# Optimization experiments

Hardware: AMD Instinct MI355X
Metric: run time of the kernel (lower is better)

## Reference

```python
import jax, jax.numpy as jnp
import numpy as np

N_EMBD = 2048
N_HEAD = 16
HEAD_DIM = N_EMBD // N_HEAD
B, T = 4, 2048
EPS = 1e-5


def layer_norm(x, w, b):
    mu = jnp.mean(x, axis=-1, keepdims=True)
    var = jnp.var(x, axis=-1, keepdims=True)
    return (x - mu) * jax.lax.rsqrt(var + EPS) * w + b


def setup_inputs() -> dict:
    key = jax.random.key(0)
    ks = jax.random.split(key, 8)
    s = 0.02
    return {
        "x": jax.random.normal(ks[0], (B, T, N_EMBD), dtype=jnp.float32),
        "ln1_w": jnp.ones((N_EMBD,), jnp.float32),
        "ln1_b": jnp.zeros((N_EMBD,), jnp.float32),
        "attn_w": jax.random.normal(ks[1], (N_EMBD, 3 * N_EMBD), jnp.float32) * s,
        "attn_b": jnp.zeros((3 * N_EMBD,), jnp.float32),
        "ln2_w": jnp.ones((N_EMBD,), jnp.float32),
        "ln2_b": jnp.zeros((N_EMBD,), jnp.float32),
        "fc_w": jax.random.normal(ks[2], (N_EMBD, 4 * N_EMBD), jnp.float32) * s,
        "fc_b": jnp.zeros((4 * N_EMBD,), jnp.float32),
        "proj_w": jax.random.normal(ks[3], (4 * N_EMBD, N_EMBD), jnp.float32) * s,
        "proj_b": jnp.zeros((N_EMBD,), jnp.float32),
    }


def reference(x, ln1_w, ln1_b, attn_w, attn_b, ln2_w, ln2_b, fc_w, fc_b, proj_w, proj_b):
    b, t, c = x.shape
    # --- causal self-attention on ln_1(x); note: source Block has NO residual
    # and attention's c_proj is never invoked in the original forward. ---
    h = layer_norm(x, ln1_w, ln1_b)
    qkv = h @ attn_w + attn_b                      # [B,T,3C]
    q, k, v = jnp.split(qkv, 3, axis=-1)
    q = q.reshape(b, t, N_HEAD, HEAD_DIM)
    k = k.reshape(b, t, N_HEAD, HEAD_DIM)
    v = v.reshape(b, t, N_HEAD, HEAD_DIM)
    scale = 1.0 / np.sqrt(HEAD_DIM).astype(np.float32)
    scores = jnp.einsum("bqhd,bkhd->bhqk", q, k) * scale   # [B,H,T,T]
    causal = jnp.tril(jnp.ones((t, t), dtype=bool))
    scores = jnp.where(causal, scores, -jnp.inf)
    attn = jax.nn.softmax(scores, axis=-1)
    y = jnp.einsum("bhqk,bkhd->bqhd", attn, v).reshape(b, t, c)
    # --- MLP on ln_2(y); again no residual in the source Block ---
    h2 = layer_norm(y, ln2_w, ln2_b)
    out = jax.nn.gelu(h2 @ fc_w + fc_b, approximate=False) @ proj_w + proj_b
    return out
```

## Files before the change

### kernel.cpp

```cpp
#include <hip/hip_runtime.h>
#include <hip/hip_bf16.h>

typedef __attribute__((ext_vector_type(8))) short      bf16x8;
typedef __attribute__((ext_vector_type(4))) float      f32x4;
typedef __attribute__((ext_vector_type(8))) unsigned short u16x8;

__device__ __forceinline__ unsigned short f2bf(float f) {
    union { __hip_bfloat16 h; unsigned short u; } cv;
    cv.h = __float2bfloat16(f);
    return cv.u;
}
__device__ __forceinline__ float bf2f(unsigned short u) {
    union { float f; unsigned int i; } cv;
    cv.i = ((unsigned int)u) << 16;
    return cv.f;
}
__device__ __forceinline__ void gload_lds16(const void* g, void* l) {
    __builtin_amdgcn_global_load_lds(
        (const __attribute__((address_space(1))) void*)g,
        (__attribute__((address_space(3))) void*)l, 16, 0, 0);
}
__device__ __forceinline__ f32x4 mfma16(bf16x8 a, bf16x8 b, f32x4 c) {
    return __builtin_amdgcn_mfma_f32_16x16x32_bf16(a, b, c, 0, 0, 0);
}
__device__ __forceinline__ float gelu_f(float x) {
    return 0.5f * x * (1.0f + erff(x * 0.70710678118654752f));
}

#define S_BARRIER() asm volatile("s_barrier" ::: "memory")
#define LGKM0()     do { asm volatile("s_waitcnt lgkmcnt(0)" ::: "memory"); \
                         __builtin_amdgcn_sched_barrier(0); } while (0)

template<int IN_BF16>
__global__ __launch_bounds__(256) void ln_kernel(const void* in, const float* w, const float* b,
                                                 unsigned short* out) {
    const int row = blockIdx.x;
    const int tid = threadIdx.x;
    float v[8];
    if constexpr (IN_BF16) {
        const unsigned short* p = (const unsigned short*)in + (size_t)row * 2048 + tid * 8;
        u16x8 raw = *(const u16x8*)p;
#pragma unroll
        for (int j = 0; j < 8; j++) v[j] = bf2f(raw[j]);
    } else {
        const float* p = (const float*)in + (size_t)row * 2048 + tid * 8;
        float4 a = ((const float4*)p)[0];
        float4 c = ((const float4*)p)[1];
        v[0] = a.x; v[1] = a.y; v[2] = a.z; v[3] = a.w;
        v[4] = c.x; v[5] = c.y; v[6] = c.z; v[7] = c.w;
    }
    float s = 0.f, ss = 0.f;
#pragma unroll
    for (int j = 0; j < 8; j++) { s += v[j]; ss += v[j] * v[j]; }
#pragma unroll
    for (int off = 32; off > 0; off >>= 1) {
        s  += __shfl_xor(s, off);
        ss += __shfl_xor(ss, off);
    }
    __shared__ float red[8];
    const int wid = tid >> 6, lane = tid & 63;
    if (lane == 0) { red[wid] = s; red[4 + wid] = ss; }
    __syncthreads();
    s  = red[0] + red[1] + red[2] + red[3];
    ss = red[4] + red[5] + red[6] + red[7];
    const float mean = s * (1.0f / 2048.0f);
    const float var  = ss * (1.0f / 2048.0f) - mean * mean;
    const float rstd = rsqrtf(var + 1e-5f);
    unsigned short* op = out + (size_t)row * 2048 + tid * 8;
    u16x8 ov;
#pragma unroll
    for (int j = 0; j < 8; j++) {
        int c = tid * 8 + j;
        ov[j] = f2bf((v[j] - mean) * rstd * w[c] + b[c]);
    }
    *(u16x8*)op = ov;
}

__global__ __launch_bounds__(256) void wt_kernel(const float* W, unsigned short* WT, int K, int N) {
    __shared__ unsigned short sm[32][33];
    const int n0 = blockIdx.x * 32, k0 = blockIdx.y * 32;
    const int tx = threadIdx.x, ty = threadIdx.y;
#pragma unroll
    for (int i = 0; i < 4; i++) {
        int k = ty + i * 8;
        sm[k][tx] = f2bf(W[(size_t)(k0 + k) * N + n0 + tx]);
    }
    __syncthreads();
#pragma unroll
    for (int i = 0; i < 4; i++) {
        int n = ty + i * 8;
        WT[(size_t)(n0 + n) * K + k0 + tx] = sm[tx][n];
    }
}

__global__ __launch_bounds__(256) void vt_kernel(const unsigned short* qkv, unsigned short* vT) {
    __shared__ unsigned short sm[32][33];
    const int t0 = blockIdx.x * 32, d0 = blockIdx.y * 32, bh = blockIdx.z;
    const int b = bh >> 4, h = bh & 15;
    const int tx = threadIdx.x, ty = threadIdx.y;
#pragma unroll
    for (int i = 0; i < 4; i++) {
        int t = ty + i * 8;
        sm[t][tx] = qkv[(size_t)(b * 2048 + t0 + t) * 6144 + 4096 + h * 128 + d0 + tx];
    }
    __syncthreads();
#pragma unroll
    for (int i = 0; i < 4; i++) {
        int d = ty + i * 8;
        vT[(size_t)(bh * 128 + d0 + d) * 2048 + t0 + tx] = sm[tx][d];
    }
}

template<int OUT_BF16, int ACT_GELU>
__global__ __launch_bounds__(512, 2) void gemm256(const unsigned short* __restrict__ A,
                                                  const unsigned short* __restrict__ BT,
                                                  const float* __restrict__ bias,
                                                  void* __restrict__ Cout,
                                                  int M, int N, int K) {
    __shared__ unsigned short As[2][256 * 64];
    __shared__ unsigned short Bs[2][256 * 64];
    const int tid = threadIdx.x;
    const int gx = gridDim.x;
    const int lin = blockIdx.y * gx + blockIdx.x;
    const int cpx = (gx * gridDim.y) >> 3;
    const int swz = (lin & 7) * cpx + (lin >> 3);
    const int n0 = (swz % gx) * 256, m0 = (swz / gx) * 256;

    const int wid = tid >> 6, lane = tid & 63;
    const int wr = wid >> 2, wc = wid & 3;
    const int lg = lane >> 4, l15 = lane & 15;
    const int nkt = K >> 6;

    const int sr = tid >> 3;
    const int scol = ((tid & 7) ^ (sr & 7)) * 8;
    const int sdst = tid * 8;

    auto stageA = [&](int ta, int h) {
        const unsigned short* g = A + (size_t)(m0 + h * 128 + sr) * K + ta * 64 + scol;
        unsigned short* d = &As[ta & 1][h * 8192 + sdst];
        gload_lds16(g, d);
        gload_lds16(g + (size_t)64 * K, d + 4096);
    };
    auto stageB = [&](int ta, int h) {
        const unsigned short* g = BT + (size_t)(n0 + h * 128 + sr) * K + ta * 64 + scol;
        unsigned short* d = &Bs[ta & 1][h * 8192 + sdst];
        gload_lds16(g, d);
        gload_lds16(g + (size_t)64 * K, d + 4096);
    };

    stageA(0, 0); stageA(0, 1); stageB(0, 0); stageB(0, 1);
    asm volatile("s_waitcnt vmcnt(0)" ::: "memory");
    S_BARRIER();

    f32x4 acc[8][4] = {};
    const int lxor = l15 & 7;
    const int co0 = (lg ^ lxor) * 8;
    const int co1 = ((4 + lg) ^ lxor) * 8;
    const int arow = wr * 128 + l15;
    const int brow = wc * 64 + l15;

#define GPHASE(MH, CO, READB, STAGE_STMT, TAIL_STMT)                              \
    do {                                                                          \
        bf16x8 af[4];                                                             \
        _Pragma("unroll")                                                         \
        for (int i = 0; i < 4; i++)                                               \
            af[i] = *(const bf16x8*)&Ap[(arow + ((MH) * 4 + i) * 16) * 64 + (CO)];\
        if (READB) {                                                              \
            _Pragma("unroll")                                                     \
            for (int n = 0; n < 4; n++)                                           \
                bq[n] = *(const bf16x8*)&Bp[(brow + n * 16) * 64 + (CO)];         \
        }                                                                         \
        STAGE_STMT;                                                               \
        S_BARRIER();                                                              \
        LGKM0();                                                                  \
        __builtin_amdgcn_s_setprio(1);                                            \
        _Pragma("unroll")                                                         \
        for (int i = 0; i < 4; i++) {                                             \
            _Pragma("unroll")                                                     \
            for (int n = 0; n < 4; n++)                                           \
                acc[(MH) * 4 + i][n] = mfma16(af[i], bq[n], acc[(MH) * 4 + i][n]);\
        }                                                                         \
        __builtin_amdgcn_s_setprio(0);                                            \
        TAIL_STMT;                                                                \
        S_BARRIER();                                                              \
    } while (0)

    for (int t = 0; t < nkt; ++t) {
        const int p = t & 1;
        const unsigned short* Ap = As[p];
        const unsigned short* Bp = Bs[p];
        bf16x8 bq[4];

        GPHASE(0, co0, 1,
               if (t + 1 < nkt) { stageA(t + 1, 0); stageA(t + 1, 1); },
               (void)0);
        GPHASE(1, co0, 0,
               if (t + 1 < nkt) { stageB(t + 1, 0); stageB(t + 1, 1); },
               (void)0);
        GPHASE(0, co1, 1, (void)0, (void)0);
        GPHASE(1, co1, 0, (void)0,
               if (t + 1 < nkt) asm volatile("s_waitcnt vmcnt(0)" ::: "memory"));
    }
#undef GPHASE

#pragma unroll
    for (int n = 0; n < 4; n++) {
        const int col = n0 + wc * 64 + n * 16 + l15;
        const float bv = bias[col];
#pragma unroll
        for (int m = 0; m < 8; m++) {
            const int rbase = m0 + wr * 128 + m * 16 + lg * 4;
#pragma unroll
            for (int r = 0; r < 4; r++) {
                float v = acc[m][n][r] + bv;
                if (ACT_GELU) v = gelu_f(v);
                if (OUT_BF16)
                    ((unsigned short*)Cout)[(size_t)(rbase + r) * N + col] = f2bf(v);
                else
                    ((float*)Cout)[(size_t)(rbase + r) * N + col] = v;
            }
        }
    }
}

__global__ __launch_bounds__(256) void attn_kernel(const unsigned short* __restrict__ qkv,
                                                   const unsigned short* __restrict__ vT,
                                                   unsigned short* __restrict__ y) {
    __shared__ unsigned short Qs[64 * 128];
    __shared__ unsigned short Ks[64 * 128];
    __shared__ unsigned short VTs[128 * 64];
    const int pair = blockIdx.x, h = blockIdx.y, b = blockIdx.z;
    const int tid = threadIdx.x, wid = tid >> 6, lane = tid & 63;
    const int lg = lane >> 4, l15 = lane & 15;
    const float scale = 0.08838834764831845f;
    unsigned short* Ps = &Qs[wid * 1024];

    for (int pass = 0; pass < 2; pass++) {
        const int qt = (pass == 0) ? (31 - pair) : pair;
        __syncthreads();
#pragma unroll
        for (int i = 0; i < 4; i++) {
            int idx = tid + 256 * i;
            int row = idx >> 4, ch = idx & 15;
            const unsigned short* g = qkv + (size_t)(b * 2048 + qt * 64 + row) * 6144
                                      + h * 128 + ((ch ^ (row & 7)) * 8);
            gload_lds16(g, &Qs[idx * 8]);
        }
        __syncthreads();
        const int rq = wid * 16 + l15;
        bf16x8 qf[4];
#pragma unroll
        for (int c = 0; c < 4; c++)
            qf[c] = *(const bf16x8*)&Qs[rq * 128 + (((c * 4 + lg) ^ (rq & 7)) * 8)];

        float m_run[4], l_run[4];
#pragma unroll
        for (int r = 0; r < 4; r++) { m_run[r] = -1e30f; l_run[r] = 0.f; }
        f32x4 O[8] = {};

        const int nkb = qt + 1;
        for (int kb = 0; kb < nkb; kb++) {
            __syncthreads();
#pragma unroll
            for (int i = 0; i < 4; i++) {
                int idx = tid + 256 * i;
                int row = idx >> 4, ch = idx & 15;
                const unsigned short* g = qkv + (size_t)(b * 2048 + kb * 64 + row) * 6144
                                          + 2048 + h * 128 + ((ch ^ (row & 7)) * 8);
                gload_lds16(g, &Ks[idx * 8]);
            }
#pragma unroll
            for (int i = 0; i < 4; i++) {
                int idx = tid + 256 * i;
                int row = idx >> 3, ch = idx & 7;
                const unsigned short* g = vT + (size_t)((b * 16 + h) * 128 + row) * 2048
                                          + kb * 64 + ((ch ^ (row & 7)) * 8);
                gload_lds16(g, &VTs[idx * 8]);
            }
            __syncthreads();

            f32x4 S[4] = {};
#pragma unroll
            for (int n = 0; n < 4; n++) {
                const int rk = n * 16 + l15;
#pragma unroll
                for (int c = 0; c < 4; c++) {
                    bf16x8 kf = *(const bf16x8*)&Ks[rk * 128 + (((c * 4 + lg) ^ (rk & 7)) * 8)];
                    S[n] = mfma16(qf[c], kf, S[n]);
                }
            }

            const int qgb = qt * 64 + wid * 16 + lg * 4;
#pragma unroll
            for (int r = 0; r < 4; r++) {
                const int qg = qgb + r;
                float sv[4];
#pragma unroll
                for (int n = 0; n < 4; n++) {
                    const int kg = kb * 64 + n * 16 + l15;
                    sv[n] = (kg <= qg) ? S[n][r] * scale : -1e30f;
                }
                float mx = fmaxf(fmaxf(sv[0], sv[1]), fmaxf(sv[2], sv[3]));
                mx = fmaxf(mx, __shfl_xor(mx, 1));
                mx = fmaxf(mx, __shfl_xor(mx, 2));
                mx = fmaxf(mx, __shfl_xor(mx, 4));
                mx = fmaxf(mx, __shfl_xor(mx, 8));
                const float mnew = fmaxf(m_run[r], mx);
                const float f = __expf(m_run[r] - mnew);
                const float p0 = __expf(sv[0] - mnew), p1 = __expf(sv[1] - mnew);
                const float p2 = __expf(sv[2] - mnew), p3 = __expf(sv[3] - mnew);
                float rs = (p0 + p1) + (p2 + p3);
                rs += __shfl_xor(rs, 1);
                rs += __shfl_xor(rs, 2);
                rs += __shfl_xor(rs, 4);
                rs += __shfl_xor(rs, 8);
                l_run[r] = l_run[r] * f + rs;
                m_run[r] = mnew;
#pragma unroll
                for (int n2 = 0; n2 < 8; n2++) O[n2][r] *= f;
                const int prow = lg * 4 + r;
                const int pxor = (prow & 7) << 3;
                Ps[(prow * 64 + l15) ^ pxor]      = f2bf(p0);
                Ps[(prow * 64 + 16 + l15) ^ pxor] = f2bf(p1);
                Ps[(prow * 64 + 32 + l15) ^ pxor] = f2bf(p2);
                Ps[(prow * 64 + 48 + l15) ^ pxor] = f2bf(p3);
            }

#pragma unroll
            for (int kk = 0; kk < 2; kk++) {
                bf16x8 pf = *(const bf16x8*)&Ps[l15 * 64 + (((kk * 4 + lg) ^ (l15 & 7)) * 8)];
#pragma unroll
                for (int n2 = 0; n2 < 8; n2++) {
                    const int rv = n2 * 16 + l15;
                    bf16x8 vf = *(const bf16x8*)&VTs[rv * 64 + (((kk * 4 + lg) ^ (rv & 7)) * 8)];
                    O[n2] = mfma16(pf, vf, O[n2]);
                }
            }
        }

#pragma unroll
        for (int r = 0; r < 4; r++) {
            const float inv = 1.0f / l_run[r];
            const size_t row = (size_t)(b * 2048 + qt * 64 + wid * 16 + lg * 4 + r);
#pragma unroll
            for (int n2 = 0; n2 < 8; n2++)
                y[row * 2048 + h * 128 + n2 * 16 + l15] = f2bf(O[n2][r] * inv);
        }
    }
}

extern "C" void kernel_launch(void* const* d_in, const int* in_sizes, int n_in,
                              void* d_out, int out_size, void* d_ws, size_t ws_size,
                              hipStream_t stream) {
    const float* x      = (const float*)d_in[0];
    const float* ln1_w  = (const float*)d_in[1];
    const float* ln1_b  = (const float*)d_in[2];
    const float* attn_w = (const float*)d_in[3];
    const float* attn_b = (const float*)d_in[4];
    const float* ln2_w  = (const float*)d_in[5];
    const float* ln2_b  = (const float*)d_in[6];
    const float* fc_w   = (const float*)d_in[7];
    const float* fc_b   = (const float*)d_in[8];
    const float* proj_w = (const float*)d_in[9];
    const float* proj_b = (const float*)d_in[10];
    float* out = (float*)d_out;

    char* ws = (char*)d_ws;
    const size_t MB = 1024ull * 1024ull;
    unsigned short* Wt   = (unsigned short*)(ws + 0);
    unsigned short* X1   = (unsigned short*)(ws + 32 * MB);
    unsigned short* X2   = (unsigned short*)(ws + 64 * MB);
    unsigned short* QKV  = (unsigned short*)(ws + 96 * MB);
    unsigned short* VT   = (unsigned short*)(ws + 192 * MB);
    unsigned short* Abuf = (unsigned short*)(ws + 96 * MB);

    ln_kernel<0><<<8192, 256, 0, stream>>>(x, ln1_w, ln1_b, X1);
    wt_kernel<<<dim3(6144 / 32, 2048 / 32), dim3(32, 8), 0, stream>>>(attn_w, Wt, 2048, 6144);
    gemm256<1, 0><<<dim3(24, 32), 512, 0, stream>>>(X1, Wt, attn_b, QKV, 8192, 6144, 2048);
    vt_kernel<<<dim3(64, 4, 64), dim3(32, 8), 0, stream>>>(QKV, VT);
    attn_kernel<<<dim3(16, 16, 4), 256, 0, stream>>>(QKV, VT, X2);
    ln_kernel<1><<<8192, 256, 0, stream>>>(X2, ln2_w, ln2_b, X1);
    wt_kernel<<<dim3(8192 / 32, 2048 / 32), dim3(32, 8), 0, stream>>>(fc_w, Wt, 2048, 8192);
    gemm256<1, 1><<<dim3(32, 32), 512, 0, stream>>>(X1, Wt, fc_b, Abuf, 8192, 8192, 2048);
    wt_kernel<<<dim3(2048 / 32, 8192 / 32), dim3(32, 8), 0, stream>>>(proj_w, Wt, 8192, 2048);
    gemm256<0, 0><<<dim3(8, 32), 512, 0, stream>>>(Abuf, Wt, proj_b, out, 8192, 2048, 8192);
}
```

Before: 1.062 ms.

## Deepen GEMM global-to-LDS prefetch to two stages with partial vmcnt waits

Restructures the GEMM main loop so that B and half of A for tile t+2 are issued early while tile t is computed. Waits now use partial vmcnt counts rather than draining to zero, which keeps more loads in flight and hides global memory latency. The per-wave A row mapping changes so each half-tile phase reads rows that were staged separately, and the phase order is reshuffled to keep two B fragment sets in registers. The extra register pressure and the subtle buffer-reuse ordering across the double-buffered LDS are risks.

```diff
diff --git a/kernel.cpp b/kernel.cpp
--- a/kernel.cpp
+++ b/kernel.cpp
@@ -149,26 +149,31 @@
     };
 
     stageA(0, 0); stageA(0, 1); stageB(0, 0); stageB(0, 1);
-    asm volatile("s_waitcnt vmcnt(0)" ::: "memory");
+    if (nkt > 1) {
+        stageB(1, 0); stageB(1, 1); stageA(1, 0);
+        asm volatile("s_waitcnt vmcnt(6)" ::: "memory");
+    } else {
+        asm volatile("s_waitcnt vmcnt(0)" ::: "memory");
+    }
     S_BARRIER();
 
     f32x4 acc[8][4] = {};
     const int lxor = l15 & 7;
     const int co0 = (lg ^ lxor) * 8;
     const int co1 = ((4 + lg) ^ lxor) * 8;
-    const int arow = wr * 128 + l15;
+    const int arow0 = wr * 64 + l15;
     const int brow = wc * 64 + l15;
 
-#define GPHASE(MH, CO, READB, STAGE_STMT, TAIL_STMT)                              \
+#define GPHASE(MH, CO, BQ, READB, STAGE_STMT, TAIL_STMT)                          \
     do {                                                                          \
         bf16x8 af[4];                                                             \
         _Pragma("unroll")                                                         \
         for (int i = 0; i < 4; i++)                                               \
-            af[i] = *(const bf16x8*)&Ap[(arow + ((MH) * 4 + i) * 16) * 64 + (CO)];\
+            af[i] = *(const bf16x8*)&Ap[((MH) * 128 + arow0 + i * 16) * 64 + (CO)];\
         if (READB) {                                                              \
             _Pragma("unroll")                                                     \
             for (int n = 0; n < 4; n++)                                           \
-                bq[n] = *(const bf16x8*)&Bp[(brow + n * 16) * 64 + (CO)];         \
+                BQ[n] = *(const bf16x8*)&Bp[(brow + n * 16) * 64 + (CO)];         \
         }                                                                         \
         STAGE_STMT;                                                               \
         S_BARRIER();                                                              \
@@ -178,7 +183,7 @@
         for (int i = 0; i < 4; i++) {                                             \
             _Pragma("unroll")                                                     \
             for (int n = 0; n < 4; n++)                                           \
-                acc[(MH) * 4 + i][n] = mfma16(af[i], bq[n], acc[(MH) * 4 + i][n]);\
+                acc[(MH) * 4 + i][n] = mfma16(af[i], BQ[n], acc[(MH) * 4 + i][n]);\
         }                                                                         \
         __builtin_amdgcn_s_setprio(0);                                            \
         TAIL_STMT;                                                                \
@@ -189,17 +194,21 @@
         const int p = t & 1;
         const unsigned short* Ap = As[p];
         const unsigned short* Bp = Bs[p];
-        bf16x8 bq[4];
-
-        GPHASE(0, co0, 1,
-               if (t + 1 < nkt) { stageA(t + 1, 0); stageA(t + 1, 1); },
+        bf16x8 bq0[4], bq1[4];
+        const bool steady = (t < nkt - 2);
+
+        GPHASE(0, co0, bq0, 1,
+               if (t + 1 < nkt) stageA(t + 1, 1),
                (void)0);
-        GPHASE(1, co0, 0,
-               if (t + 1 < nkt) { stageB(t + 1, 0); stageB(t + 1, 1); },
+        GPHASE(0, co1, bq1, 1, (void)0,
+               if (steady) asm volatile("s_waitcnt vmcnt(8)" ::: "memory");
+               else        asm volatile("s_waitcnt vmcnt(0)" ::: "memory"));
+        GPHASE(1, co0, bq0, 0,
+               if (t + 2 < nkt) { stageB(t + 2, 0); stageB(t + 2, 1); stageA(t + 2, 0); },
                (void)0);
-        GPHASE(0, co1, 1, (void)0, (void)0);
-        GPHASE(1, co1, 0, (void)0,
-               if (t + 1 < nkt) asm volatile("s_waitcnt vmcnt(0)" ::: "memory"));
+        GPHASE(1, co1, bq1, 0, (void)0,
+               if (steady) asm volatile("s_waitcnt vmcnt(8)" ::: "memory");
+               else        asm volatile("s_waitcnt vmcnt(0)" ::: "memory"));
     }
 #undef GPHASE
 
@@ -209,7 +218,7 @@
         const float bv = bias[col];
 #pragma unroll
         for (int m = 0; m < 8; m++) {
-            const int rbase = m0 + wr * 128 + m * 16 + lg * 4;
+            const int rbase = m0 + (m >> 2) * 128 + wr * 64 + (m & 3) * 16 + lg * 4;
 #pragma unroll
             for (int r = 0; r < 4; r++) {
                 float v = acc[m][n][r] + bv;
```

Measured after the change: 1.072 ms. About the same (+1.0%).

## Restructure GEMM main loop into finer-grained staged prefetch with partial vmcnt waits

Applied to the files above, without the earlier changes.

Rewrites the GEMM k-loop to process two k-tiles per iteration, spreading the global-to-LDS stage loads for the next tile across eight sub-phases. It starts the following B half early and waits only until at most two loads are outstanding (vmcnt(2)) instead of draining all loads. The aim is better overlap of memory traffic with MFMA work and shorter barrier stalls. It also changes the LDS addressing (aoff/boff) and the warp-to-tile mapping. It assumes nkt is even, and the partial waits and early stage issue raise the risk of ordering bugs.

```diff
diff --git a/kernel.cpp b/kernel.cpp
--- a/kernel.cpp
+++ b/kernel.cpp
@@ -27,9 +27,7 @@
     return 0.5f * x * (1.0f + erff(x * 0.70710678118654752f));
 }
 
-#define S_BARRIER() asm volatile("s_barrier" ::: "memory")
-#define LGKM0()     do { asm volatile("s_waitcnt lgkmcnt(0)" ::: "memory"); \
-                         __builtin_amdgcn_sched_barrier(0); } while (0)
+#define VMCNT(N)  asm volatile("s_waitcnt vmcnt(" #N ")" ::: "memory")
 
 template<int IN_BF16>
 __global__ __launch_bounds__(256) void ln_kernel(const void* in, const float* w, const float* b,
@@ -149,59 +147,70 @@
     };
 
     stageA(0, 0); stageA(0, 1); stageB(0, 0); stageB(0, 1);
-    asm volatile("s_waitcnt vmcnt(0)" ::: "memory");
-    S_BARRIER();
+    stageB(1, 0);
+    VMCNT(2);
+    __builtin_amdgcn_s_barrier();
 
     f32x4 acc[8][4] = {};
     const int lxor = l15 & 7;
     const int co0 = (lg ^ lxor) * 8;
     const int co1 = ((4 + lg) ^ lxor) * 8;
-    const int arow = wr * 128 + l15;
-    const int brow = wc * 64 + l15;
-
-#define GPHASE(MH, CO, READB, STAGE_STMT, TAIL_STMT)                              \
-    do {                                                                          \
-        bf16x8 af[4];                                                             \
-        _Pragma("unroll")                                                         \
-        for (int i = 0; i < 4; i++)                                               \
-            af[i] = *(const bf16x8*)&Ap[(arow + ((MH) * 4 + i) * 16) * 64 + (CO)];\
-        if (READB) {                                                              \
-            _Pragma("unroll")                                                     \
-            for (int n = 0; n < 4; n++)                                           \
-                bq[n] = *(const bf16x8*)&Bp[(brow + n * 16) * 64 + (CO)];         \
-        }                                                                         \
-        STAGE_STMT;                                                               \
-        S_BARRIER();                                                              \
-        LGKM0();                                                                  \
-        __builtin_amdgcn_s_setprio(1);                                            \
-        _Pragma("unroll")                                                         \
-        for (int i = 0; i < 4; i++) {                                             \
-            _Pragma("unroll")                                                     \
-            for (int n = 0; n < 4; n++)                                           \
-                acc[(MH) * 4 + i][n] = mfma16(af[i], bq[n], acc[(MH) * 4 + i][n]);\
-        }                                                                         \
-        __builtin_amdgcn_s_setprio(0);                                            \
-        TAIL_STMT;                                                                \
-        S_BARRIER();                                                              \
-    } while (0)
-
-    for (int t = 0; t < nkt; ++t) {
-        const int p = t & 1;
-        const unsigned short* Ap = As[p];
-        const unsigned short* Bp = Bs[p];
-        bf16x8 bq[4];
-
-        GPHASE(0, co0, 1,
-               if (t + 1 < nkt) { stageA(t + 1, 0); stageA(t + 1, 1); },
-               (void)0);
-        GPHASE(1, co0, 0,
-               if (t + 1 < nkt) { stageB(t + 1, 0); stageB(t + 1, 1); },
-               (void)0);
-        GPHASE(0, co1, 1, (void)0, (void)0);
-        GPHASE(1, co1, 0, (void)0,
-               if (t + 1 < nkt) asm volatile("s_waitcnt vmcnt(0)" ::: "memory"));
-    }
-#undef GPHASE
+    const int aoff = wr * 8192;
+    const int boff = (wc >> 1) * 8192 + (wc & 1) * 4096;
+
+#define RD_A(P, MB, CO)                                                          \
+    _Pragma("unroll") for (int i = 0; i < 4; i++)                                \
+        af[i] = *(const bf16x8*)&P[aoff + (((MB) + i) * 16 + l15) * 64 + (CO)];
+#define RD_B(DST, P, CO)                                                         \
+    _Pragma("unroll") for (int n = 0; n < 4; n++)                                \
+        DST[n] = *(const bf16x8*)&P[boff + (n * 16 + l15) * 64 + (CO)];
+#define MM(MB, BQ)                                                               \
+    __builtin_amdgcn_s_setprio(1);                                               \
+    _Pragma("unroll") for (int i = 0; i < 4; i++)                                \
+        _Pragma("unroll") for (int n = 0; n < 4; n++)                            \
+            acc[(MB) + i][n] = mfma16(af[i], BQ[n], acc[(MB) + i][n]);           \
+    __builtin_amdgcn_s_setprio(0);
+#define BAR()  __builtin_amdgcn_s_barrier()
+#define LGKM() asm volatile("s_waitcnt lgkmcnt(0)" ::: "memory")
+
+    for (int it = 0, nit = nkt >> 1; it < nit; ++it) {
+        const int T0 = it * 2, T1 = T0 + 1;
+        const unsigned short* Ae = As[0];
+        const unsigned short* Be = Bs[0];
+        const unsigned short* Ao = As[1];
+        const unsigned short* Bo = Bs[1];
+        bf16x8 af[4], bq0[4], bq1[4];
+
+        RD_A(Ae, 0, co0); RD_B(bq0, Be, co0);
+        stageB(T1, 1);
+        BAR(); LGKM(); MM(0, bq0); BAR();
+        RD_A(Ae, 4, co0);
+        stageA(T1, 0);
+        BAR(); LGKM(); MM(4, bq0); BAR();
+        RD_A(Ae, 0, co1); RD_B(bq1, Be, co1);
+        stageA(T1, 1);
+        BAR(); LGKM(); MM(0, bq1); BAR();
+        RD_A(Ae, 4, co1);
+        if (T0 + 2 < nkt) stageB(T0 + 2, 0);
+        BAR(); LGKM(); MM(4, bq1); VMCNT(2); BAR();
+        RD_A(Ao, 0, co0); RD_B(bq0, Bo, co0);
+        if (T0 + 2 < nkt) stageB(T0 + 2, 1);
+        BAR(); LGKM(); MM(0, bq0); BAR();
+        RD_A(Ao, 4, co0);
+        if (T0 + 2 < nkt) stageA(T0 + 2, 0);
+        BAR(); LGKM(); MM(4, bq0); BAR();
+        RD_A(Ao, 0, co1); RD_B(bq1, Bo, co1);
+        if (T0 + 2 < nkt) stageA(T0 + 2, 1);
+        BAR(); LGKM(); MM(0, bq1); BAR();
+        RD_A(Ao, 4, co1);
+        if (T1 + 2 < nkt) stageB(T1 + 2, 0);
+        BAR(); LGKM(); MM(4, bq1); VMCNT(2); BAR();
+    }
+#undef RD_A
+#undef RD_B
+#undef MM
+#undef BAR
+#undef LGKM
 
 #pragma unroll
     for (int n = 0; n < 4; n++) {
```

Result: no change. 1.075 ms (+1.3%).
